# Kernel optimization log

Hardware: AMD Instinct MI355X
Metric: run time of the kernel (lower is better)

Reference implementation:

```python
import jax, jax.numpy as jnp
import numpy as np

L = 2048           # lattice side
R = 2.777          # public-goods multiplier r
GAMMA = 0.8
ETA = 0.8
K_FERMI = 0.5      # fermi temperature used in fermiUpdate


def _plus_sum(x):
    """3x3 plus-kernel conv with circular (wrap) padding == self + 4 rolled neighbors."""
    return (x
            + jnp.roll(x, 1, 0) + jnp.roll(x, -1, 0)
            + jnp.roll(x, 1, 1) + jnp.roll(x, -1, 1))


def setup_inputs() -> dict:
    key = jax.random.key(0)
    k1, k2, k3, k4, k5 = jax.random.split(key, 5)
    return {
        "type_t_minus": jax.random.randint(k1, (L, L), 0, 2, dtype=jnp.int32),
        "type_t": jax.random.randint(k2, (L, L), 0, 2, dtype=jnp.int32),
        "Q_tensor": jax.random.normal(k3, (L * L, 2, 2), dtype=jnp.float32),
        "learning_direction": jax.random.randint(k4, (L, L), 0, 4, dtype=jnp.int32),
        "learning_probabilities": jax.random.uniform(k5, (L, L), dtype=jnp.float32),
    }


def reference(type_t_minus, type_t, Q_tensor, learning_direction, learning_probabilities):
    N = L * L
    # ---- calculation_value: per-cell payoff from the 5 overlapping PGG games ----
    c = (type_t == 1).astype(jnp.float32)   # cooperator mask
    d = (type_t == 0).astype(jnp.float32)   # defector mask
    coop_num = _plus_sum(c)                  # cooperators in own 5-cell group
    base = coop_num * (R / 5.0)
    profit = _plus_sum(base - 1.0) * c + _plus_sum(base) * d   # [L, L]

    # ---- updateQMatrix: Q[C, A, B] <- (1-eta)*Q[C,A,B] + eta*(profit + gamma*max_b Q[C,B,b]) ----
    A = type_t_minus.reshape(-1)             # previous action, [N]
    B = type_t.reshape(-1)                   # current action,  [N]
    Qb = jnp.take_along_axis(Q_tensor, B[:, None, None], axis=1)[:, 0, :]  # Q[C, B, :] -> [N, 2]
    max_values = Qb.max(axis=1)              # [N]
    flatQ = Q_tensor.reshape(N, 4)
    idx = A * 2 + B                          # flattened (A, B) index
    old = jnp.take_along_axis(flatQ, idx[:, None], axis=1)[:, 0]
    upd = (1.0 - ETA) * old + ETA * (profit.reshape(-1) + GAMMA * max_values)
    Q_new = flatQ.at[jnp.arange(N), idx].set(upd).reshape(N, 2, 2)

    # ---- fermiUpdate: gather just-updated Q[C,A,B] (== upd), compare with 4 neighbors ----
    pm = upd.reshape(L, L)                   # fermi profit matrix

    def W(shift, axis):
        return 1.0 / (1.0 + jnp.exp((pm - jnp.roll(pm, shift, axis)) / K_FERMI))

    Ws = jnp.stack([W(1, 1), W(-1, 1), W(1, 0), W(-1, 0)])        # left,right,up,down [4,L,L]
    nb = jnp.stack([jnp.roll(type_t, 1, 1), jnp.roll(type_t, -1, 1),
                    jnp.roll(type_t, 1, 0), jnp.roll(type_t, -1, 0)])
    W_sel = jnp.take_along_axis(Ws, learning_direction[None], axis=0)[0]
    nb_sel = jnp.take_along_axis(nb, learning_direction[None], axis=0)[0]
    type_t1 = jnp.where(learning_probabilities <= W_sel, nb_sel, type_t)  # [L, L] int32

    return (Q_new, type_t1, profit)
```

## Files before the change

kernel.cpp:

```cpp
#include <hip/hip_runtime.h>


#define LSIDE 2048
#define LMASK 2047
#define LSHIFT 11
#define NCELL (LSIDE * LSIDE)

#define CROWS 4
#define TROWS 10
#define TCOLS 264
#define TI4   66
#define NI4   (TROWS * TI4)
#define BROWS 8
#define BCOLS 260
#define TILE_INTS (TROWS * TCOLS)
#define LDS_INTS  (TILE_INTS + BROWS * BCOLS)

typedef __attribute__((address_space(1))) const int gas_int;
typedef __attribute__((address_space(3))) int las_int;

__global__ __launch_bounds__(256) void spgg_fused(
    const int* __restrict__ tmin,
    const int* __restrict__ tt,
    const float* __restrict__ Q,
    const int* __restrict__ ldir,
    const float* __restrict__ lp,
    float* __restrict__ Qn,
    float* __restrict__ prof,
    float* __restrict__ t1out)
{
    __shared__ __align__(16) int lds_raw[LDS_INTS];
    int   (*tile)[TCOLS]  = reinterpret_cast<int(*)[TCOLS]>(lds_raw);
    float (*btile)[BCOLS] = reinterpret_cast<float(*)[BCOLS]>(lds_raw + TILE_INTS);

    const int t   = threadIdx.x;
    const int blk = blockIdx.x;
    const int i0  = (blk >> 3) << 2;
    const int j0  = (blk & 7) << 8;
    const int j   = j0 + t;
    const int idx0 = (i0 << LSHIFT) + j;

    int    dirm[CROWS];
    float  pvm[CROWS];
    float4 qrm[CROWS];
    int    Am[CROWS];
    #pragma unroll
    for (int m = 0; m < CROWS; ++m) {
        int idx = idx0 + (m << LSHIFT);
        dirm[m] = ldir[idx];
        pvm[m]  = lp[idx];
        qrm[m]  = ((const float4*)Q)[idx];
        Am[m]   = tmin[idx];
    }

    #pragma unroll
    for (int it = 0; it < 3; ++it) {
        int k = t + (it << 8);
        int r = k / TI4;
        int m4 = k - r * TI4;
        int row_g = (i0 + r - 3) & LMASK;
        int col_g = (j0 - 4 + (m4 << 2)) & LMASK;
        __builtin_amdgcn_global_load_lds(
            (gas_int*)&tt[(row_g << LSHIFT) + col_g],
            (las_int*)&lds_raw[k << 2], 16, 0, 0);
    }

    __syncthreads();

    const float KB        = 0.5554f;
    const float ETA       = 0.8f;
    const float ONE_M_ETA = 0.2f;
    const float GAMMA     = 0.8f;

    auto bval = [&](int tr, int tc) -> float {
        int cn = tile[tr][tc] + tile[tr-1][tc] + tile[tr+1][tc]
               + tile[tr][tc-1] + tile[tr][tc+1];
        return __fmul_rn((float)cn, KB);
    };
    #pragma unroll
    for (int r = 0; r < BROWS; ++r)
        btile[r][t] = bval(r + 1, t + 2);
    if (t < BCOLS - 256) {
        #pragma unroll
        for (int r = 0; r < BROWS; ++r)
            btile[r][256 + t] = bval(r + 1, 258 + t);
    }
    __syncthreads();

    int di[CROWS], dj[CROWS];
    float4 qn4[CROWS];
    int    An[CROWS];
    #pragma unroll
    for (int m = 0; m < CROWS; ++m) {
        di[m] = (dirm[m] == 3) - (dirm[m] == 2);
        dj[m] = (dirm[m] == 1) - (dirm[m] == 0);
        int nidx = ((((i0 + m + di[m]) & LMASK)) << LSHIFT) + ((j + dj[m]) & LMASK);
        qn4[m] = ((const float4*)Q)[nidx];
        An[m]  = tmin[nidx];
    }

    auto profit_from_b = [&](int r, int c, int coop) -> float {
        float b_c = btile[r][c];
        float b_u = btile[r-1][c];
        float b_d = btile[r+1][c];
        float b_l = btile[r][c-1];
        float b_r = btile[r][c+1];
        float s0 = __fadd_rn(__fadd_rn(__fadd_rn(__fadd_rn(b_c, b_u), b_d), b_l), b_r);
        float s1 = __fadd_rn(__fadd_rn(__fadd_rn(__fadd_rn(
                       __fsub_rn(b_c, 1.0f), __fsub_rn(b_u, 1.0f)),
                       __fsub_rn(b_d, 1.0f)), __fsub_rn(b_l, 1.0f)),
                       __fsub_rn(b_r, 1.0f));
        return coop ? s1 : s0;
    };

    auto upd_of = [&](float profit, float4 q4, int Ai, int Bi) -> float {
        float q0 = (Bi == 0) ? q4.x : q4.z;
        float q1 = (Bi == 0) ? q4.y : q4.w;
        float mx = fmaxf(q0, q1);
        int k = Ai * 2 + Bi;
        float old = (k == 0) ? q4.x : ((k == 1) ? q4.y : ((k == 2) ? q4.z : q4.w));
        float t0 = __fmul_rn(GAMMA, mx);
        float t1 = __fadd_rn(profit, t0);
        float t2 = __fmul_rn(ETA, t1);
        float t3 = __fmul_rn(ONE_M_ETA, old);
        return __fadd_rn(t3, t2);
    };

    int   B[CROWS];
    float updv[CROWS];
    #pragma unroll
    for (int m = 0; m < CROWS; ++m) {
        B[m] = tile[m + 3][t + 4];
        float p_own = profit_from_b(m + 2, t + 2, B[m]);
        updv[m] = upd_of(p_own, qrm[m], Am[m], B[m]);
        int idx = idx0 + (m << LSHIFT);
        int k = Am[m] * 2 + B[m];
        float4 qo;
        qo.x = (k == 0) ? updv[m] : qrm[m].x;
        qo.y = (k == 1) ? updv[m] : qrm[m].y;
        qo.z = (k == 2) ? updv[m] : qrm[m].z;
        qo.w = (k == 3) ? updv[m] : qrm[m].w;
        ((float4*)Qn)[idx] = qo;
        prof[idx] = p_own;
    }

    float e2[CROWS];
    int   Bn[CROWS];
    #pragma unroll
    for (int m = 0; m < CROWS; ++m) {
        Bn[m] = tile[m + 3 + di[m]][t + 4 + dj[m]];
        float p_nb   = profit_from_b(m + 2 + di[m], t + 2 + dj[m], Bn[m]);
        float upd_nb = upd_of(p_nb, qn4[m], An[m], Bn[m]);
        float e1 = __fsub_rn(updv[m], upd_nb);
        e2[m] = __fmul_rn(e1, 2.0f);
    }
    #pragma unroll
    for (int m = 0; m < CROWS; ++m) {
        float ex = (float)exp((double)e2[m]);
        float W  = __fdiv_rn(1.0f, __fadd_rn(1.0f, ex));
        int sel = (pvm[m] <= W) ? Bn[m] : B[m];
        t1out[idx0 + (m << LSHIFT)] = (float)sel;
    }
}

extern "C" void kernel_launch(void* const* d_in, const int* in_sizes, int n_in,
                              void* d_out, int out_size, void* d_ws, size_t ws_size,
                              hipStream_t stream) {
    const int*   type_t_minus = (const int*)d_in[0];
    const int*   type_t       = (const int*)d_in[1];
    const float* Q_tensor     = (const float*)d_in[2];
    const int*   ldir         = (const int*)d_in[3];
    const float* lprob        = (const float*)d_in[4];

    float* out   = (float*)d_out;
    float* Qn    = out;
    float* t1out = out + (size_t)4 * NCELL;
    float* prof  = out + (size_t)5 * NCELL;

    const int threads = 256;
    const int blocks  = NCELL / (threads * CROWS);
    spgg_fused<<<blocks, threads, 0, stream>>>(type_t_minus, type_t, Q_tensor,
                                               ldir, lprob, Qn, prof, t1out);
}
```

Baseline: 213.2 us.

## Give each wavefront a private LDS tile to drop block-level barriers

Each 64-lane wavefront now loads its own 10x72 halo tile of type_t through registers into a private LDS region and computes its own base tile. This replaces the block-wide global_load_lds plus __syncthreads with plain lgkmcnt waits. The neighbor Q/tmin gathers are also issued before the tile wait so their latency overlaps. In exchange there is more redundant halo loading and computation per wave. The code also relies on wave-synchronous LDS visibility without an explicit barrier.

```diff
diff --git a/kernel.cpp b/kernel.cpp
--- a/kernel.cpp
+++ b/kernel.cpp
@@ -7,17 +7,14 @@
 #define NCELL (LSIDE * LSIDE)
 
 #define CROWS 4
-#define TROWS 10
-#define TCOLS 264
-#define TI4   66
-#define NI4   (TROWS * TI4)
-#define BROWS 8
-#define BCOLS 260
-#define TILE_INTS (TROWS * TCOLS)
-#define LDS_INTS  (TILE_INTS + BROWS * BCOLS)
-
-typedef __attribute__((address_space(1))) const int gas_int;
-typedef __attribute__((address_space(3))) int las_int;
+#define TR 10
+#define TC 72
+#define BR 8
+#define BC 68
+#define TILE_INTS (TR * TC)
+#define BT_INTS   (BR * BC)
+#define WREG      (TILE_INTS + BT_INTS)
+#define NI4       180
 
 __global__ __launch_bounds__(256) void spgg_fused(
     const int* __restrict__ tmin,
@@ -29,21 +26,21 @@
     float* __restrict__ prof,
     float* __restrict__ t1out)
 {
-    __shared__ __align__(16) int lds_raw[LDS_INTS];
-    int   (*tile)[TCOLS]  = reinterpret_cast<int(*)[TCOLS]>(lds_raw);
-    float (*btile)[BCOLS] = reinterpret_cast<float(*)[BCOLS]>(lds_raw + TILE_INTS);
+    __shared__ __align__(16) int lds_raw[4 * WREG];
 
-    const int t   = threadIdx.x;
-    const int blk = blockIdx.x;
-    const int i0  = (blk >> 3) << 2;
-    const int j0  = (blk & 7) << 8;
-    const int j   = j0 + t;
+    const int tid  = threadIdx.x;
+    const int lane = tid & 63;
+    const int wid  = tid >> 6;
+    int*   wtile = lds_raw + wid * WREG;
+    float* wbt   = (float*)(wtile + TILE_INTS);
+
+    const int blk  = blockIdx.x;
+    const int i0   = (blk >> 3) << 2;
+    const int j0w  = ((blk & 7) << 8) + (wid << 6);
+    const int j    = j0w + lane;
     const int idx0 = (i0 << LSHIFT) + j;
 
-    int    dirm[CROWS];
-    float  pvm[CROWS];
-    float4 qrm[CROWS];
-    int    Am[CROWS];
+    int dirm[CROWS]; float pvm[CROWS]; float4 qrm[CROWS]; int Am[CROWS];
     #pragma unroll
     for (int m = 0; m < CROWS; ++m) {
         int idx = idx0 + (m << LSHIFT);
@@ -53,58 +50,66 @@
         Am[m]   = tmin[idx];
     }
 
-    #pragma unroll
-    for (int it = 0; it < 3; ++it) {
-        int k = t + (it << 8);
-        int r = k / TI4;
-        int m4 = k - r * TI4;
-        int row_g = (i0 + r - 3) & LMASK;
-        int col_g = (j0 - 4 + (m4 << 2)) & LMASK;
-        __builtin_amdgcn_global_load_lds(
-            (gas_int*)&tt[(row_g << LSHIFT) + col_g],
-            (las_int*)&lds_raw[k << 2], 16, 0, 0);
+    {
+        auto srcp = [&](int k) -> const int4* {
+            int r  = k / 18;
+            int c4 = k - r * 18;
+            int row_g = (i0 + r - 3) & LMASK;
+            int col_g = (j0w - 4 + (c4 << 2)) & LMASK;
+            return (const int4*)&tt[(row_g << LSHIFT) + col_g];
+        };
+        const int k0 = lane, k1 = 64 + lane, k2 = 128 + lane;
+        int4 v0 = *srcp(k0);
+        int4 v1 = *srcp(k1);
+        int4 v2;
+        const bool has2 = (k2 < NI4);
+        if (has2) v2 = *srcp(k2);
+        *(int4*)&wtile[k0 << 2] = v0;
+        *(int4*)&wtile[k1 << 2] = v1;
+        if (has2) *(int4*)&wtile[k2 << 2] = v2;
     }
 
-    __syncthreads();
+    int di[CROWS], dj[CROWS]; float4 qn4[CROWS]; int An[CROWS];
+    #pragma unroll
+    for (int m = 0; m < CROWS; ++m) {
+        di[m] = (dirm[m] == 3) - (dirm[m] == 2);
+        dj[m] = (dirm[m] == 1) - (dirm[m] == 0);
+        int nidx = (((i0 + m + di[m]) & LMASK) << LSHIFT) + ((j + dj[m]) & LMASK);
+        qn4[m] = ((const float4*)Q)[nidx];
+        An[m]  = tmin[nidx];
+    }
+
+    asm volatile("s_waitcnt lgkmcnt(0)" ::: "memory");
 
     const float KB        = 0.5554f;
     const float ETA       = 0.8f;
     const float ONE_M_ETA = 0.2f;
     const float GAMMA     = 0.8f;
 
-    auto bval = [&](int tr, int tc) -> float {
-        int cn = tile[tr][tc] + tile[tr-1][tc] + tile[tr+1][tc]
-               + tile[tr][tc-1] + tile[tr][tc+1];
-        return __fmul_rn((float)cn, KB);
+    auto bcol = [&](int c) {
+        const int tc = c + 2;
+        int a[TR];
+        #pragma unroll
+        for (int r = 0; r < TR; ++r) a[r] = wtile[r * TC + tc];
+        #pragma unroll
+        for (int r = 0; r < BR; ++r) {
+            int cn = a[r + 1] + a[r] + a[r + 2]
+                   + wtile[(r + 1) * TC + tc - 1]
+                   + wtile[(r + 1) * TC + tc + 1];
+            wbt[r * BC + c] = __fmul_rn((float)cn, KB);
+        }
     };
-    #pragma unroll
-    for (int r = 0; r < BROWS; ++r)
-        btile[r][t] = bval(r + 1, t + 2);
-    if (t < BCOLS - 256) {
-        #pragma unroll
-        for (int r = 0; r < BROWS; ++r)
-            btile[r][256 + t] = bval(r + 1, 258 + t);
-    }
-    __syncthreads();
+    bcol(lane);
+    if (lane < BC - 64) bcol(64 + lane);
 
-    int di[CROWS], dj[CROWS];
-    float4 qn4[CROWS];
-    int    An[CROWS];
-    #pragma unroll
-    for (int m = 0; m < CROWS; ++m) {
-        di[m] = (dirm[m] == 3) - (dirm[m] == 2);
-        dj[m] = (dirm[m] == 1) - (dirm[m] == 0);
-        int nidx = ((((i0 + m + di[m]) & LMASK)) << LSHIFT) + ((j + dj[m]) & LMASK);
-        qn4[m] = ((const float4*)Q)[nidx];
-        An[m]  = tmin[nidx];
-    }
+    asm volatile("s_waitcnt lgkmcnt(0)" ::: "memory");
 
     auto profit_from_b = [&](int r, int c, int coop) -> float {
-        float b_c = btile[r][c];
-        float b_u = btile[r-1][c];
-        float b_d = btile[r+1][c];
-        float b_l = btile[r][c-1];
-        float b_r = btile[r][c+1];
+        float b_c = wbt[r * BC + c];
+        float b_u = wbt[(r - 1) * BC + c];
+        float b_d = wbt[(r + 1) * BC + c];
+        float b_l = wbt[r * BC + c - 1];
+        float b_r = wbt[r * BC + c + 1];
         float s0 = __fadd_rn(__fadd_rn(__fadd_rn(__fadd_rn(b_c, b_u), b_d), b_l), b_r);
         float s1 = __fadd_rn(__fadd_rn(__fadd_rn(__fadd_rn(
                        __fsub_rn(b_c, 1.0f), __fsub_rn(b_u, 1.0f)),
@@ -130,8 +135,8 @@
     float updv[CROWS];
     #pragma unroll
     for (int m = 0; m < CROWS; ++m) {
-        B[m] = tile[m + 3][t + 4];
-        float p_own = profit_from_b(m + 2, t + 2, B[m]);
+        B[m] = wtile[(m + 3) * TC + lane + 4];
+        float p_own = profit_from_b(m + 2, lane + 2, B[m]);
         updv[m] = upd_of(p_own, qrm[m], Am[m], B[m]);
         int idx = idx0 + (m << LSHIFT);
         int k = Am[m] * 2 + B[m];
@@ -148,8 +153,8 @@
     int   Bn[CROWS];
     #pragma unroll
     for (int m = 0; m < CROWS; ++m) {
-        Bn[m] = tile[m + 3 + di[m]][t + 4 + dj[m]];
-        float p_nb   = profit_from_b(m + 2 + di[m], t + 2 + dj[m], Bn[m]);
+        Bn[m] = wtile[(m + 3 + di[m]) * TC + lane + 4 + dj[m]];
+        float p_nb   = profit_from_b(m + 2 + di[m], lane + 2 + dj[m], Bn[m]);
         float upd_nb = upd_of(p_nb, qn4[m], An[m], Bn[m]);
         float e1 = __fsub_rn(updv[m], upd_nb);
         e2[m] = __fmul_rn(e1, 2.0f);
```

Result: no change. 212.3 us (-0.4%).
